# Kernel optimization log

Measured on AMD Instinct MI355X. Metric: run time of the kernel, lower is better.

The kernel has to match this reference:

```python
import jax, jax.numpy as jnp
import numpy as np

IN_C, HID, L, NN, BS, OUT = 32, 128, 4, 64, 512, 3
N = NN * BS  # total graph vertices
EPS_LN = 1e-5
EPS_SM = 1e-16  # PyG softmax eps


def setup_inputs() -> dict:
    key = jax.random.key(0)
    ks = jax.random.split(key, 16)
    E = 524288
    x = jax.random.normal(ks[0], (N, IN_C), dtype=jnp.float32)
    edge_index = jax.random.randint(ks[1], (2, E), 0, N, dtype=jnp.int64)
    s = 0.1
    # first GAT layer (in -> hidden)
    W0 = jax.random.normal(ks[2], (IN_C, HID), dtype=jnp.float32) * s
    att_src0 = jax.random.normal(ks[3], (HID,), dtype=jnp.float32) * s
    att_dst0 = jax.random.normal(ks[4], (HID,), dtype=jnp.float32) * s
    bias0 = jnp.zeros((HID,), dtype=jnp.float32)
    # residual GAT layers (hidden -> hidden), stacked over L
    W_res = jax.random.normal(ks[5], (L, HID, HID), dtype=jnp.float32) * s
    att_src_res = jax.random.normal(ks[6], (L, HID), dtype=jnp.float32) * s
    att_dst_res = jax.random.normal(ks[7], (L, HID), dtype=jnp.float32) * s
    bias_res = jnp.zeros((L, HID), dtype=jnp.float32)
    gamma = jnp.ones((L, HID), dtype=jnp.float32)
    beta = jnp.zeros((L, HID), dtype=jnp.float32)
    # per-node predictor heads
    W1p = jax.random.normal(ks[8], (NN, HID, HID // 2), dtype=jnp.float32) * s
    W2p = jax.random.normal(ks[9], (NN, HID // 2, OUT), dtype=jnp.float32) * s
    return {"x": x, "edge_index": edge_index, "W0": W0, "att_src0": att_src0,
            "att_dst0": att_dst0, "bias0": bias0, "W_res": W_res,
            "att_src_res": att_src_res, "att_dst_res": att_dst_res,
            "bias_res": bias_res, "gamma": gamma, "beta": beta,
            "W1p": W1p, "W2p": W2p}


def _gat(x, src, dst, W, a_src, a_dst, b):
    # PyG GATConv, heads=1, negative_slope=0.2, self-loops already appended
    h = x @ W                                   # [N, H]
    a_s = (h * a_src).sum(-1)                   # [N]
    a_d = (h * a_dst).sum(-1)                   # [N]
    e = jax.nn.leaky_relu(a_s[src] + a_d[dst], 0.2)   # [E]
    m = jax.ops.segment_max(e, dst, num_segments=N)
    e = jnp.exp(e - m[dst])
    z = jax.ops.segment_sum(e, dst, num_segments=N)
    alpha = e / (z[dst] + EPS_SM)               # [E]
    out = jax.ops.segment_sum(h[src] * alpha[:, None], dst, num_segments=N)
    return out + b


def _layernorm(x, g, b):
    mu = x.mean(-1, keepdims=True)
    var = ((x - mu) ** 2).mean(-1, keepdims=True)
    return (x - mu) * jax.lax.rsqrt(var + EPS_LN) * g + b


def reference(x, edge_index, W0, att_src0, att_dst0, bias0, W_res,
              att_src_res, att_dst_res, bias_res, gamma, beta, W1p, W2p):
    loops = jnp.arange(N, dtype=edge_index.dtype)
    src = jnp.concatenate([edge_index[0], loops])
    dst = jnp.concatenate([edge_index[1], loops])
    # first GAT + relu
    h = jax.nn.relu(_gat(x, src, dst, W0, att_src0, att_dst0, bias0))
    # res+ blocks: h = h + conv(dropout(act(norm(h))))  (dropout=identity, eval)
    for i in range(L):
        t = jax.nn.relu(_layernorm(h, gamma[i], beta[i]))
        t = _gat(t, src, dst, W_res[i], att_src_res[i], att_dst_res[i], bias_res[i])
        h = h + t
    h = jax.nn.relu(_layernorm(h, gamma[0], beta[0]))
    # per-node predictor heads
    h = h.reshape(NN, BS, HID)
    t = jax.nn.relu(jnp.einsum('nbh,nhk->nbk', h, W1p))
    logits = jnp.einsum('nbk,nko->nbo', t, W2p)
    return jax.nn.softmax(logits, axis=-1)   # softmax over class dim (dim=1 per node slice)
```

## Files before the change

### kernel.cpp

```cpp
#include <hip/hip_runtime.h>
#include <math.h>

#define NND   32768
#define HIDD  128
#define NHEAD 64
#define BSS   512
#define OUTC  3

typedef _Float16 half_t;
typedef __attribute__((ext_vector_type(8))) _Float16 half8;
typedef __attribute__((ext_vector_type(4))) float f32x4;

__global__ void count_kernel(const int* __restrict__ ei, int E,
                             int* __restrict__ counts, int* __restrict__ rank) {
    int j = blockIdx.x * 256 + threadIdx.x;
    int Etot = E + NND;
    if (j >= Etot) return;
    int dst = (j < E) ? ei[E + j] : (j - E);
    rank[j] = atomicAdd(&counts[dst], 1);
}

__global__ __launch_bounds__(1024) void scan_kernel(const int* __restrict__ counts,
                                                    int* __restrict__ off) {
    __shared__ int sums[1024];
    int tid = threadIdx.x;
    int base = tid * 32;
    int tmp[32];
    int run = 0;
#pragma unroll
    for (int i = 0; i < 8; ++i) {
        int4 c4 = *(const int4*)&counts[base + i * 4];
        tmp[i*4+0] = run; run += c4.x;
        tmp[i*4+1] = run; run += c4.y;
        tmp[i*4+2] = run; run += c4.z;
        tmp[i*4+3] = run; run += c4.w;
    }
    sums[tid] = run;
    __syncthreads();
    for (int d = 1; d < 1024; d <<= 1) {
        int v = (tid >= d) ? sums[tid - d] : 0;
        __syncthreads();
        sums[tid] += v;
        __syncthreads();
    }
    int ebase = (tid == 0) ? 0 : sums[tid - 1];
#pragma unroll
    for (int i = 0; i < 32; ++i) off[base + i] = ebase + tmp[i];
    if (tid == 1023) off[NND] = sums[1023];
}

__global__ void fill_kernel(const int* __restrict__ ei, int E,
                            const int* __restrict__ off, const int* __restrict__ rank,
                            int* __restrict__ csr_src) {
    int j = blockIdx.x * 256 + threadIdx.x;
    int Etot = E + NND;
    if (j >= Etot) return;
    int src, dst;
    if (j < E) { src = ei[j]; dst = ei[E + j]; }
    else       { src = j - E; dst = j - E; }
    csr_src[off[dst] + rank[j]] = src;
}

__global__ __launch_bounds__(256) void prep_kernel(const float* __restrict__ W_res,
                                                   const float* __restrict__ W1p,
                                                   half_t* __restrict__ Wh,
                                                   half_t* __restrict__ W1h) {
    __shared__ float tile[32][33];
    int b = blockIdx.x;
    const float* src; half_t* dst; int srcld, k0, n0;
    if (b < 64) {
        int l = b >> 4, t = b & 15;
        k0 = (t >> 2) * 32; n0 = (t & 3) * 32;
        src = W_res + (size_t)l * 128 * 128; srcld = 128;
        dst = Wh + (size_t)l * 128 * 128;
    } else {
        int bb = b - 64; int head = bb >> 3, t = bb & 7;
        k0 = (t >> 1) * 32; n0 = (t & 1) * 32;
        src = W1p + (size_t)head * 128 * 64; srcld = 64;
        dst = W1h + (size_t)head * 64 * 128;
    }
    int c = threadIdx.x & 31, r0 = threadIdx.x >> 5;
#pragma unroll
    for (int i = 0; i < 4; ++i) {
        int r = r0 + i * 8;
        tile[r][c] = src[(size_t)(k0 + r) * srcld + n0 + c];
    }
    __syncthreads();
#pragma unroll
    for (int i = 0; i < 4; ++i) {
        int rr = r0 + i * 8;
        dst[(size_t)(n0 + rr) * 128 + k0 + c] = (half_t)tile[c][rr];
    }
}

template <int K, int KT>
__global__ __launch_bounds__(256) void gemm_kernel(const float* __restrict__ X,
                                                   const float* __restrict__ W,
                                                   const float* __restrict__ att_src,
                                                   const float* __restrict__ att_dst,
                                                   half_t* __restrict__ Gh,
                                                   float* __restrict__ a_s,
                                                   float* __restrict__ a_d) {
    __shared__ float Ws[KT * HIDD];
    __shared__ float Xs[K * 32];
    int tid = threadIdx.x;
    int n0 = blockIdx.x * 32;
    for (int i = tid; i < 32 * K; i += 256) {
        int n = i / K, k = i - n * K;
        Xs[k * 32 + n] = X[(size_t)(n0 + n) * K + k];
    }
    int cg = (tid & 31) * 4;
    int ng = (tid >> 5) * 4;
    float acc[4][4] = {};
    for (int kt = 0; kt < K; kt += KT) {
        __syncthreads();
        for (int i = tid; i < KT * HIDD / 4; i += 256)
            ((float4*)Ws)[i] = ((const float4*)W)[(size_t)kt * (HIDD / 4) + i];
        __syncthreads();
#pragma unroll 4
        for (int k = 0; k < KT; ++k) {
            float4 wv = *(const float4*)&Ws[k * HIDD + cg];
            float4 xv = *(const float4*)&Xs[(kt + k) * 32 + ng];
            acc[0][0] += xv.x * wv.x; acc[0][1] += xv.x * wv.y; acc[0][2] += xv.x * wv.z; acc[0][3] += xv.x * wv.w;
            acc[1][0] += xv.y * wv.x; acc[1][1] += xv.y * wv.y; acc[1][2] += xv.y * wv.z; acc[1][3] += xv.y * wv.w;
            acc[2][0] += xv.z * wv.x; acc[2][1] += xv.z * wv.y; acc[2][2] += xv.z * wv.z; acc[2][3] += xv.z * wv.w;
            acc[3][0] += xv.w * wv.x; acc[3][1] += xv.w * wv.y; acc[3][2] += xv.w * wv.z; acc[3][3] += xv.w * wv.w;
        }
    }
    float4 asv = *(const float4*)&att_src[cg];
    float4 adv = *(const float4*)&att_dst[cg];
#pragma unroll
    for (int i = 0; i < 4; ++i) {
        int n = n0 + ng + i;
        union { int2 i2; half_t h[4]; } u;
        u.h[0] = (half_t)acc[i][0]; u.h[1] = (half_t)acc[i][1];
        u.h[2] = (half_t)acc[i][2]; u.h[3] = (half_t)acc[i][3];
        *(int2*)&Gh[(size_t)n * HIDD + cg] = u.i2;
        float ps = acc[i][0]*asv.x + acc[i][1]*asv.y + acc[i][2]*asv.z + acc[i][3]*asv.w;
        float pd = acc[i][0]*adv.x + acc[i][1]*adv.y + acc[i][2]*adv.z + acc[i][3]*adv.w;
#pragma unroll
        for (int o = 16; o; o >>= 1) { ps += __shfl_xor(ps, o); pd += __shfl_xor(pd, o); }
        if ((tid & 31) == 0) { a_s[n] = ps; a_d[n] = pd; }
    }
}

__global__ __launch_bounds__(256) void gemm_mfma_kernel(const half_t* __restrict__ Th,
                                                        const half_t* __restrict__ Whl,
                                                        const float* __restrict__ att_src,
                                                        const float* __restrict__ att_dst,
                                                        half_t* __restrict__ Gh,
                                                        float* __restrict__ a_s,
                                                        float* __restrict__ a_d) {
    __shared__ half_t Wt[128 * 136];
    __shared__ half_t OutT[64 * HIDD];
    int tid = threadIdx.x;
    int n0 = blockIdx.x * 64;
    for (int i = tid; i < 128 * 16; i += 256) {
        int n = i >> 4, c = i & 15;
        *(int4*)&Wt[n * 136 + c * 8] = *(const int4*)&Whl[(size_t)n * 128 + c * 8];
    }
    int wv = tid >> 6, lane = tid & 63;
    int q = lane >> 4, r15 = lane & 15;
    half8 afrag[4];
    int nodeA = n0 + wv * 16 + r15;
#pragma unroll
    for (int s = 0; s < 4; ++s)
        afrag[s] = *(const half8*)&Th[(size_t)nodeA * HIDD + s * 32 + q * 8];
    __syncthreads();
    f32x4 acc[8];
#pragma unroll
    for (int ct = 0; ct < 8; ++ct) {
        f32x4 c = {0.f, 0.f, 0.f, 0.f};
        int n = ct * 16 + r15;
#pragma unroll
        for (int s = 0; s < 4; ++s) {
            half8 b = *(const half8*)&Wt[n * 136 + s * 32 + q * 8];
            c = __builtin_amdgcn_mfma_f32_16x16x32_f16(afrag[s], b, c, 0, 0, 0);
        }
        acc[ct] = c;
    }
    float ps[4] = {0.f,0.f,0.f,0.f}, pd[4] = {0.f,0.f,0.f,0.f};
#pragma unroll
    for (int ct = 0; ct < 8; ++ct) {
        float av = att_src[ct * 16 + r15];
        float bv = att_dst[ct * 16 + r15];
#pragma unroll
        for (int r = 0; r < 4; ++r) {
            float v = acc[ct][r];
            ps[r] += v * av;
            pd[r] += v * bv;
            OutT[(wv * 16 + q * 4 + r) * HIDD + ct * 16 + r15] = (half_t)v;
        }
    }
#pragma unroll
    for (int o = 8; o; o >>= 1) {
#pragma unroll
        for (int r = 0; r < 4; ++r) { ps[r] += __shfl_xor(ps[r], o); pd[r] += __shfl_xor(pd[r], o); }
    }
    if (r15 == 0) {
#pragma unroll
        for (int r = 0; r < 4; ++r) {
            int node = n0 + wv * 16 + q * 4 + r;
            a_s[node] = ps[r];
            a_d[node] = pd[r];
        }
    }
    __syncthreads();
    const int4* srcp = (const int4*)OutT;
    int4* dstp = (int4*)&Gh[(size_t)n0 * HIDD];
    for (int i = tid; i < 64 * HIDD * 2 / 16; i += 256)
        dstp[i] = srcp[i];
}

__global__ __launch_bounds__(256) void agg_kernel(const half_t* __restrict__ Gh,
                                                  const float* __restrict__ a_s,
                                                  const float* __restrict__ a_dv,
                                                  const int* __restrict__ csr_src,
                                                  const int* __restrict__ off,
                                                  const float* __restrict__ bias,
                                                  const float* __restrict__ gamma,
                                                  const float* __restrict__ beta,
                                                  float* __restrict__ Hbuf,
                                                  half_t* __restrict__ Th,
                                                  int mode) {
    int d = (blockIdx.x * 256 + threadIdx.x) >> 6;
    int lane = threadIdx.x & 63;
    if (d >= NND) return;
    int q = lane >> 4, r15 = lane & 15;
    int beg = off[d], end = off[d + 1];
    float adv = a_dv[d];
    float pz = 0.f;
    float acc[8] = {0.f,0.f,0.f,0.f,0.f,0.f,0.f,0.f};
    for (int base = beg; base < end; base += 64) {
        int j = base + lane;
        int s = 0; float p = 0.f;
        if (j < end) {
            s = csr_src[j];
            float t = a_s[s] + adv;
            t = (t > 0.f) ? t : 0.2f * t;
            p = __expf(t);
        }
        pz += p;
        int cnt = end - base; if (cnt > 64) cnt = 64;
        for (int k4 = 0; k4 < cnt; k4 += 16) {
            int   s0 = __shfl(s, k4 + q);       float p0 = __shfl(p, k4 + q);
            int   s1 = __shfl(s, k4 + 4 + q);   float p1 = __shfl(p, k4 + 4 + q);
            int   s2 = __shfl(s, k4 + 8 + q);   float p2 = __shfl(p, k4 + 8 + q);
            int   s3 = __shfl(s, k4 + 12 + q);  float p3 = __shfl(p, k4 + 12 + q);
            half8 h0 = *(const half8*)&Gh[(size_t)s0 * HIDD + r15 * 8];
            half8 h1 = *(const half8*)&Gh[(size_t)s1 * HIDD + r15 * 8];
            half8 h2 = *(const half8*)&Gh[(size_t)s2 * HIDD + r15 * 8];
            half8 h3 = *(const half8*)&Gh[(size_t)s3 * HIDD + r15 * 8];
#pragma unroll
            for (int i = 0; i < 8; ++i) acc[i] += p0 * (float)h0[i];
#pragma unroll
            for (int i = 0; i < 8; ++i) acc[i] += p1 * (float)h1[i];
#pragma unroll
            for (int i = 0; i < 8; ++i) acc[i] += p2 * (float)h2[i];
#pragma unroll
            for (int i = 0; i < 8; ++i) acc[i] += p3 * (float)h3[i];
        }
    }
#pragma unroll
    for (int o = 32; o; o >>= 1) pz += __shfl_xor(pz, o);
#pragma unroll
    for (int i = 0; i < 8; ++i) {
        acc[i] += __shfl_xor(acc[i], 16);
        acc[i] += __shfl_xor(acc[i], 32);
    }
    float inv = 1.f / (pz + 1e-16f);
    float4 b0 = *(const float4*)&bias[r15 * 8];
    float4 b1 = *(const float4*)&bias[r15 * 8 + 4];
    float h[8];
    h[0] = acc[0]*inv + b0.x; h[1] = acc[1]*inv + b0.y; h[2] = acc[2]*inv + b0.z; h[3] = acc[3]*inv + b0.w;
    h[4] = acc[4]*inv + b1.x; h[5] = acc[5]*inv + b1.y; h[6] = acc[6]*inv + b1.z; h[7] = acc[7]*inv + b1.w;
    if (mode == 0) {
#pragma unroll
        for (int i = 0; i < 8; ++i) h[i] = fmaxf(h[i], 0.f);
    } else {
        float4 o0 = *(const float4*)&Hbuf[(size_t)d * HIDD + r15 * 8];
        float4 o1 = *(const float4*)&Hbuf[(size_t)d * HIDD + r15 * 8 + 4];
        h[0] += o0.x; h[1] += o0.y; h[2] += o0.z; h[3] += o0.w;
        h[4] += o1.x; h[5] += o1.y; h[6] += o1.z; h[7] += o1.w;
    }
    float sum = 0.f;
#pragma unroll
    for (int i = 0; i < 8; ++i) sum += h[i];
#pragma unroll
    for (int o = 8; o; o >>= 1) sum += __shfl_xor(sum, o);
    float mu = sum * (1.f / HIDD);
    float var = 0.f;
#pragma unroll
    for (int i = 0; i < 8; ++i) { float dx = h[i] - mu; var += dx * dx; }
#pragma unroll
    for (int o = 8; o; o >>= 1) var += __shfl_xor(var, o);
    float rs = rsqrtf(var * (1.f / HIDD) + 1e-5f);
    float4 g0 = *(const float4*)&gamma[r15 * 8];
    float4 g1 = *(const float4*)&gamma[r15 * 8 + 4];
    float4 bb0 = *(const float4*)&beta[r15 * 8];
    float4 bb1 = *(const float4*)&beta[r15 * 8 + 4];
    float gg[8] = {g0.x,g0.y,g0.z,g0.w,g1.x,g1.y,g1.z,g1.w};
    float be[8] = {bb0.x,bb0.y,bb0.z,bb0.w,bb1.x,bb1.y,bb1.z,bb1.w};
    if (q == 0) {
        *(float4*)&Hbuf[(size_t)d * HIDD + r15 * 8]     = make_float4(h[0], h[1], h[2], h[3]);
        *(float4*)&Hbuf[(size_t)d * HIDD + r15 * 8 + 4] = make_float4(h[4], h[5], h[6], h[7]);
        union { int4 v; half_t hh[8]; } u;
#pragma unroll
        for (int i = 0; i < 8; ++i)
            u.hh[i] = (half_t)fmaxf((h[i] - mu) * rs * gg[i] + be[i], 0.f);
        *(int4*)&Th[(size_t)d * HIDD + r15 * 8] = u.v;
    }
}

__global__ __launch_bounds__(256) void pred_kernel(const half_t* __restrict__ Th,
                                                   const half_t* __restrict__ W1h,
                                                   const float* __restrict__ W2p,
                                                   float* __restrict__ out) {
    __shared__ half_t W1t[64 * 136];
    __shared__ float W2s[64 * OUTC];
    int tid = threadIdx.x;
    int head = blockIdx.x >> 2;
    int part = blockIdx.x & 3;
    const half_t* W1g = W1h + (size_t)head * 64 * 128;
    for (int i = tid; i < 64 * 16; i += 256) {
        int n = i >> 4, c = i & 15;
        *(int4*)&W1t[n * 136 + c * 8] = *(const int4*)&W1g[(size_t)n * 128 + c * 8];
    }
    if (tid < 64 * OUTC) W2s[tid] = W2p[(size_t)head * 64 * OUTC + tid];
    __syncthreads();
    int wv = tid >> 6, lane = tid & 63;
    int q = lane >> 4, r15 = lane & 15;
#pragma unroll
    for (int t16 = 0; t16 < 2; ++t16) {
        int rowbase = part * 128 + wv * 32 + t16 * 16;
        int nodeA = head * BSS + rowbase + r15;
        half8 afrag[4];
#pragma unroll
        for (int s = 0; s < 4; ++s)
            afrag[s] = *(const half8*)&Th[(size_t)nodeA * HIDD + s * 32 + q * 8];
        float lg[3][4];
#pragma unroll
        for (int o = 0; o < 3; ++o)
#pragma unroll
            for (int r = 0; r < 4; ++r) lg[o][r] = 0.f;
#pragma unroll
        for (int ct = 0; ct < 4; ++ct) {
            f32x4 c = {0.f, 0.f, 0.f, 0.f};
#pragma unroll
            for (int s = 0; s < 4; ++s) {
                half8 b = *(const half8*)&W1t[(ct * 16 + r15) * 136 + s * 32 + q * 8];
                c = __builtin_amdgcn_mfma_f32_16x16x32_f16(afrag[s], b, c, 0, 0, 0);
            }
            float w2a = W2s[(ct * 16 + r15) * OUTC + 0];
            float w2b = W2s[(ct * 16 + r15) * OUTC + 1];
            float w2c = W2s[(ct * 16 + r15) * OUTC + 2];
#pragma unroll
            for (int r = 0; r < 4; ++r) {
                float t = fmaxf(c[r], 0.f);
                lg[0][r] += t * w2a;
                lg[1][r] += t * w2b;
                lg[2][r] += t * w2c;
            }
        }
#pragma unroll
        for (int o = 8; o; o >>= 1)
#pragma unroll
            for (int oo = 0; oo < 3; ++oo)
#pragma unroll
                for (int r = 0; r < 4; ++r) lg[oo][r] += __shfl_xor(lg[oo][r], o);
        if (r15 == 0) {
#pragma unroll
            for (int r = 0; r < 4; ++r) {
                int row = rowbase + q * 4 + r;
                float l0 = lg[0][r], l1 = lg[1][r], l2 = lg[2][r];
                float mx = fmaxf(l0, fmaxf(l1, l2));
                float e0 = __expf(l0 - mx), e1 = __expf(l1 - mx), e2 = __expf(l2 - mx);
                float inv = 1.f / (e0 + e1 + e2);
                float* op = out + (size_t)(head * BSS + row) * OUTC;
                op[0] = e0 * inv; op[1] = e1 * inv; op[2] = e2 * inv;
            }
        }
    }
}

extern "C" void kernel_launch(void* const* d_in, const int* in_sizes, int n_in,
                              void* d_out, int out_size, void* d_ws, size_t ws_size,
                              hipStream_t stream) {
    const float* x        = (const float*)d_in[0];
    const int*   ei       = (const int*)d_in[1];
    const float* W0       = (const float*)d_in[2];
    const float* att_src0 = (const float*)d_in[3];
    const float* att_dst0 = (const float*)d_in[4];
    const float* bias0    = (const float*)d_in[5];
    const float* W_res    = (const float*)d_in[6];
    const float* as_res   = (const float*)d_in[7];
    const float* ad_res   = (const float*)d_in[8];
    const float* b_res    = (const float*)d_in[9];
    const float* gamma    = (const float*)d_in[10];
    const float* beta     = (const float*)d_in[11];
    const float* W1p      = (const float*)d_in[12];
    const float* W2p      = (const float*)d_in[13];
    float* out = (float*)d_out;

    int E = in_sizes[1] / 2;
    int Etot = E + NND;

    char* p = (char*)d_ws;
    auto alloc = [&](size_t bytes) { void* r = (void*)p; p += (bytes + 255) & ~(size_t)255; return r; };
    int*    counts  = (int*)alloc((size_t)NND * 4);
    int*    off     = (int*)alloc((size_t)(NND + 1) * 4);
    int*    rank    = (int*)alloc((size_t)Etot * 4);
    int*    csr_src = (int*)alloc((size_t)Etot * 4);
    half_t* Gh      = (half_t*)alloc((size_t)NND * HIDD * 2);
    half_t* Th      = (half_t*)alloc((size_t)NND * HIDD * 2);
    float*  Hbuf    = (float*)alloc((size_t)NND * HIDD * 4);
    float*  a_s     = (float*)alloc((size_t)NND * 4);
    float*  a_d     = (float*)alloc((size_t)NND * 4);
    half_t* Wh      = (half_t*)alloc((size_t)4 * HIDD * HIDD * 2);
    half_t* W1h     = (half_t*)alloc((size_t)NHEAD * 64 * HIDD * 2);

    int egrid = (Etot + 255) / 256;

    hipMemsetAsync(counts, 0, (size_t)NND * 4, stream);
    count_kernel<<<egrid, 256, 0, stream>>>(ei, E, counts, rank);
    scan_kernel<<<1, 1024, 0, stream>>>(counts, off);
    fill_kernel<<<egrid, 256, 0, stream>>>(ei, E, off, rank, csr_src);
    prep_kernel<<<576, 256, 0, stream>>>(W_res, W1p, Wh, W1h);

    gemm_kernel<32, 32><<<NND / 32, 256, 0, stream>>>(x, W0, att_src0, att_dst0, Gh, a_s, a_d);
    agg_kernel<<<NND / 4, 256, 0, stream>>>(Gh, a_s, a_d, csr_src, off, bias0,
                                            gamma, beta, Hbuf, Th, 0);

    for (int i = 0; i < 4; ++i) {
        gemm_mfma_kernel<<<NND / 64, 256, 0, stream>>>(Th, Wh + (size_t)i * HIDD * HIDD,
                                                       as_res + i * HIDD, ad_res + i * HIDD,
                                                       Gh, a_s, a_d);
        int gi = (i < 3) ? (i + 1) : 0;
        agg_kernel<<<NND / 4, 256, 0, stream>>>(Gh, a_s, a_d, csr_src, off, b_res + i * HIDD,
                                                gamma + gi * HIDD, beta + gi * HIDD, Hbuf, Th, 1);
    }

    pred_kernel<<<dim3(NHEAD * 4), 256, 0, stream>>>(Th, W1h, W2p, out);
}
```

Before: 329.8 us.

## Aggregate before transform in GAT layers and precompute attention vectors W·att

Each GAT layer is reordered to aggregate the raw input features over neighbours first and then multiply by W, which is valid because the attention logits can be computed from the input using precomputed W·att vectors. For the first layer this gathers 32-wide fp16 inputs instead of 128-wide transformed features. LayerNorm, ReLU, the residual add and the next layer's attention logits are fused into the GEMM epilogue, and the predictor head is fused into the last GEMM. The fp16 input copy, the W·att products and the count zeroing move into a single prep kernel. The softmax is computed without max subtraction, which risks overflow for large logits, and fp16 rounding now happens at different points.

After: 302.5 us. 1.09x faster.

```diff
diff --git a/kernel.cpp b/kernel.cpp
--- a/kernel.cpp
+++ b/kernel.cpp
@@ -10,6 +10,94 @@
 typedef _Float16 half_t;
 typedef __attribute__((ext_vector_type(8))) _Float16 half8;
 typedef __attribute__((ext_vector_type(4))) float f32x4;
+
+__global__ __launch_bounds__(256) void prep_kernel(const float* __restrict__ W0,
+        const float* __restrict__ W_res, const float* __restrict__ W1p,
+        const float* __restrict__ as0, const float* __restrict__ ad0,
+        const float* __restrict__ as_res, const float* __restrict__ ad_res,
+        const float* __restrict__ x,
+        half_t* __restrict__ Wh, half_t* __restrict__ W1h, half_t* __restrict__ W0t,
+        float* __restrict__ wvec, half_t* __restrict__ xh, int* __restrict__ counts) {
+    int b = blockIdx.x, tid = threadIdx.x;
+    if (b < 64) {
+        __shared__ float tile[32][33];
+        int l = b >> 4, t = b & 15;
+        int k0 = (t >> 2) * 32, n0 = (t & 3) * 32;
+        const float* src = W_res + (size_t)l * 128 * 128;
+        half_t* dst = Wh + (size_t)l * 128 * 128;
+        int c = tid & 31, r0 = tid >> 5;
+#pragma unroll
+        for (int i = 0; i < 4; ++i) tile[r0 + i * 8][c] = src[(size_t)(k0 + r0 + i * 8) * 128 + n0 + c];
+        __syncthreads();
+#pragma unroll
+        for (int i = 0; i < 4; ++i) dst[(size_t)(n0 + r0 + i * 8) * 128 + k0 + c] = (half_t)tile[c][r0 + i * 8];
+    } else if (b < 576) {
+        __shared__ float tile[32][33];
+        int bb = b - 64, head = bb >> 3, t = bb & 7;
+        int k0 = (t >> 1) * 32, n0 = (t & 1) * 32;
+        const float* src = W1p + (size_t)head * 128 * 64;
+        half_t* dst = W1h + (size_t)head * 64 * 128;
+        int c = tid & 31, r0 = tid >> 5;
+#pragma unroll
+        for (int i = 0; i < 4; ++i) tile[r0 + i * 8][c] = src[(size_t)(k0 + r0 + i * 8) * 64 + n0 + c];
+        __syncthreads();
+#pragma unroll
+        for (int i = 0; i < 4; ++i) dst[(size_t)(n0 + r0 + i * 8) * 128 + k0 + c] = (half_t)tile[c][r0 + i * 8];
+    } else if (b == 576) {
+        __shared__ float t0[32][129];
+        for (int i = tid; i < 4096; i += 256) t0[i >> 7][i & 127] = W0[i];
+        __syncthreads();
+        for (int i = tid; i < 4096; i += 256) { int n = i >> 5, k = i & 31; W0t[n * 32 + k] = (half_t)t0[k][n]; }
+    } else if (b == 577) {
+        for (int task = tid; task < 1088; task += 256) {
+            const float* row; const float* att; int slot, sd;
+            if (task < 64) {
+                int k = task >> 1; sd = task & 1;
+                row = W0 + k * 128; att = sd ? ad0 : as0; slot = k;
+            } else {
+                int tt = task - 64; int l = 1 + tt / 256; int r = tt % 256;
+                int k = r >> 1; sd = r & 1;
+                row = W_res + (size_t)(l - 1) * 16384 + k * 128;
+                att = (sd ? ad_res : as_res) + (l - 1) * 128;
+                slot = l * 128 + k;
+            }
+            float s = 0.f;
+            for (int n = 0; n < 128; ++n) s += row[n] * att[n];
+            (sd ? wvec + 640 : wvec)[slot] = s;
+        }
+    } else if (b < 1090) {
+        int b2 = b - 578;
+        const float* xs = x + (size_t)b2 * 64 * 32;
+        half_t* xd = xh + (size_t)b2 * 64 * 32;
+        for (int i = tid; i < 1024; i += 256) {
+            float2 v = ((const float2*)xs)[i];
+            union { unsigned u; half_t h[2]; } cv;
+            cv.h[0] = (half_t)v.x; cv.h[1] = (half_t)v.y;
+            ((unsigned*)xd)[i] = cv.u;
+        }
+    } else {
+        int b3 = b - 1090;
+        ((int4*)counts)[b3 * 256 + tid] = make_int4(0, 0, 0, 0);
+    }
+}
+
+__global__ __launch_bounds__(256) void a0_kernel(const half_t* __restrict__ xh,
+                                                 const float* __restrict__ wvec,
+                                                 float* __restrict__ a_s, float* __restrict__ a_d) {
+    __shared__ float ws0[32], wd0[32];
+    int tid = threadIdx.x;
+    if (tid < 32) { ws0[tid] = wvec[tid]; wd0[tid] = wvec[640 + tid]; }
+    __syncthreads();
+    int g = blockIdx.x * 256 + tid;
+    int node = g >> 2, part = g & 3;
+    half8 xv = *(const half8*)&xh[(size_t)node * 32 + part * 8];
+    float s = 0.f, d2 = 0.f;
+#pragma unroll
+    for (int j = 0; j < 8; ++j) { float f = (float)xv[j]; s += f * ws0[part * 8 + j]; d2 += f * wd0[part * 8 + j]; }
+    s += __shfl_xor(s, 1); s += __shfl_xor(s, 2);
+    d2 += __shfl_xor(d2, 1); d2 += __shfl_xor(d2, 2);
+    if (part == 0) { a_s[node] = s; a_d[node] = d2; }
+}
 
 __global__ void count_kernel(const int* __restrict__ ei, int E,
                              int* __restrict__ counts, int* __restrict__ rank) {
@@ -61,171 +149,67 @@
     csr_src[off[dst] + rank[j]] = src;
 }
 
-__global__ __launch_bounds__(256) void prep_kernel(const float* __restrict__ W_res,
-                                                   const float* __restrict__ W1p,
-                                                   half_t* __restrict__ Wh,
-                                                   half_t* __restrict__ W1h) {
-    __shared__ float tile[32][33];
-    int b = blockIdx.x;
-    const float* src; half_t* dst; int srcld, k0, n0;
-    if (b < 64) {
-        int l = b >> 4, t = b & 15;
-        k0 = (t >> 2) * 32; n0 = (t & 3) * 32;
-        src = W_res + (size_t)l * 128 * 128; srcld = 128;
-        dst = Wh + (size_t)l * 128 * 128;
-    } else {
-        int bb = b - 64; int head = bb >> 3, t = bb & 7;
-        k0 = (t >> 1) * 32; n0 = (t & 1) * 32;
-        src = W1p + (size_t)head * 128 * 64; srcld = 64;
-        dst = W1h + (size_t)head * 64 * 128;
-    }
-    int c = threadIdx.x & 31, r0 = threadIdx.x >> 5;
-#pragma unroll
-    for (int i = 0; i < 4; ++i) {
-        int r = r0 + i * 8;
-        tile[r][c] = src[(size_t)(k0 + r) * srcld + n0 + c];
-    }
-    __syncthreads();
-#pragma unroll
-    for (int i = 0; i < 4; ++i) {
-        int rr = r0 + i * 8;
-        dst[(size_t)(n0 + rr) * 128 + k0 + c] = (half_t)tile[c][rr];
-    }
-}
-
-template <int K, int KT>
-__global__ __launch_bounds__(256) void gemm_kernel(const float* __restrict__ X,
-                                                   const float* __restrict__ W,
-                                                   const float* __restrict__ att_src,
-                                                   const float* __restrict__ att_dst,
-                                                   half_t* __restrict__ Gh,
-                                                   float* __restrict__ a_s,
-                                                   float* __restrict__ a_d) {
-    __shared__ float Ws[KT * HIDD];
-    __shared__ float Xs[K * 32];
-    int tid = threadIdx.x;
-    int n0 = blockIdx.x * 32;
-    for (int i = tid; i < 32 * K; i += 256) {
-        int n = i / K, k = i - n * K;
-        Xs[k * 32 + n] = X[(size_t)(n0 + n) * K + k];
-    }
-    int cg = (tid & 31) * 4;
-    int ng = (tid >> 5) * 4;
-    float acc[4][4] = {};
-    for (int kt = 0; kt < K; kt += KT) {
-        __syncthreads();
-        for (int i = tid; i < KT * HIDD / 4; i += 256)
-            ((float4*)Ws)[i] = ((const float4*)W)[(size_t)kt * (HIDD / 4) + i];
-        __syncthreads();
-#pragma unroll 4
-        for (int k = 0; k < KT; ++k) {
-            float4 wv = *(const float4*)&Ws[k * HIDD + cg];
-            float4 xv = *(const float4*)&Xs[(kt + k) * 32 + ng];
-            acc[0][0] += xv.x * wv.x; acc[0][1] += xv.x * wv.y; acc[0][2] += xv.x * wv.z; acc[0][3] += xv.x * wv.w;
-            acc[1][0] += xv.y * wv.x; acc[1][1] += xv.y * wv.y; acc[1][2] += xv.y * wv.z; acc[1][3] += xv.y * wv.w;
-            acc[2][0] += xv.z * wv.x; acc[2][1] += xv.z * wv.y; acc[2][2] += xv.z * wv.z; acc[2][3] += xv.z * wv.w;
-            acc[3][0] += xv.w * wv.x; acc[3][1] += xv.w * wv.y; acc[3][2] += xv.w * wv.z; acc[3][3] += xv.w * wv.w;
-        }
-    }
-    float4 asv = *(const float4*)&att_src[cg];
-    float4 adv = *(const float4*)&att_dst[cg];
-#pragma unroll
-    for (int i = 0; i < 4; ++i) {
-        int n = n0 + ng + i;
-        union { int2 i2; half_t h[4]; } u;
-        u.h[0] = (half_t)acc[i][0]; u.h[1] = (half_t)acc[i][1];
-        u.h[2] = (half_t)acc[i][2]; u.h[3] = (half_t)acc[i][3];
-        *(int2*)&Gh[(size_t)n * HIDD + cg] = u.i2;
-        float ps = acc[i][0]*asv.x + acc[i][1]*asv.y + acc[i][2]*asv.z + acc[i][3]*asv.w;
-        float pd = acc[i][0]*adv.x + acc[i][1]*adv.y + acc[i][2]*adv.z + acc[i][3]*adv.w;
-#pragma unroll
-        for (int o = 16; o; o >>= 1) { ps += __shfl_xor(ps, o); pd += __shfl_xor(pd, o); }
-        if ((tid & 31) == 0) { a_s[n] = ps; a_d[n] = pd; }
-    }
-}
-
-__global__ __launch_bounds__(256) void gemm_mfma_kernel(const half_t* __restrict__ Th,
-                                                        const half_t* __restrict__ Whl,
-                                                        const float* __restrict__ att_src,
-                                                        const float* __restrict__ att_dst,
-                                                        half_t* __restrict__ Gh,
-                                                        float* __restrict__ a_s,
-                                                        float* __restrict__ a_d) {
-    __shared__ half_t Wt[128 * 136];
-    __shared__ half_t OutT[64 * HIDD];
-    int tid = threadIdx.x;
-    int n0 = blockIdx.x * 64;
-    for (int i = tid; i < 128 * 16; i += 256) {
-        int n = i >> 4, c = i & 15;
-        *(int4*)&Wt[n * 136 + c * 8] = *(const int4*)&Whl[(size_t)n * 128 + c * 8];
-    }
-    int wv = tid >> 6, lane = tid & 63;
-    int q = lane >> 4, r15 = lane & 15;
-    half8 afrag[4];
-    int nodeA = n0 + wv * 16 + r15;
-#pragma unroll
-    for (int s = 0; s < 4; ++s)
-        afrag[s] = *(const half8*)&Th[(size_t)nodeA * HIDD + s * 32 + q * 8];
-    __syncthreads();
-    f32x4 acc[8];
-#pragma unroll
-    for (int ct = 0; ct < 8; ++ct) {
-        f32x4 c = {0.f, 0.f, 0.f, 0.f};
-        int n = ct * 16 + r15;
-#pragma unroll
-        for (int s = 0; s < 4; ++s) {
-            half8 b = *(const half8*)&Wt[n * 136 + s * 32 + q * 8];
-            c = __builtin_amdgcn_mfma_f32_16x16x32_f16(afrag[s], b, c, 0, 0, 0);
-        }
-        acc[ct] = c;
-    }
-    float ps[4] = {0.f,0.f,0.f,0.f}, pd[4] = {0.f,0.f,0.f,0.f};
-#pragma unroll
-    for (int ct = 0; ct < 8; ++ct) {
-        float av = att_src[ct * 16 + r15];
-        float bv = att_dst[ct * 16 + r15];
-#pragma unroll
-        for (int r = 0; r < 4; ++r) {
-            float v = acc[ct][r];
-            ps[r] += v * av;
-            pd[r] += v * bv;
-            OutT[(wv * 16 + q * 4 + r) * HIDD + ct * 16 + r15] = (half_t)v;
-        }
-    }
-#pragma unroll
-    for (int o = 8; o; o >>= 1) {
-#pragma unroll
-        for (int r = 0; r < 4; ++r) { ps[r] += __shfl_xor(ps[r], o); pd[r] += __shfl_xor(pd[r], o); }
-    }
-    if (r15 == 0) {
-#pragma unroll
-        for (int r = 0; r < 4; ++r) {
-            int node = n0 + wv * 16 + q * 4 + r;
-            a_s[node] = ps[r];
-            a_d[node] = pd[r];
-        }
-    }
-    __syncthreads();
-    const int4* srcp = (const int4*)OutT;
-    int4* dstp = (int4*)&Gh[(size_t)n0 * HIDD];
-    for (int i = tid; i < 64 * HIDD * 2 / 16; i += 256)
-        dstp[i] = srcp[i];
-}
-
-__global__ __launch_bounds__(256) void agg_kernel(const half_t* __restrict__ Gh,
-                                                  const float* __restrict__ a_s,
-                                                  const float* __restrict__ a_dv,
-                                                  const int* __restrict__ csr_src,
-                                                  const int* __restrict__ off,
-                                                  const float* __restrict__ bias,
-                                                  const float* __restrict__ gamma,
-                                                  const float* __restrict__ beta,
-                                                  float* __restrict__ Hbuf,
-                                                  half_t* __restrict__ Th,
-                                                  int mode) {
+__global__ __launch_bounds__(256) void agg0_kernel(const half_t* __restrict__ xh,
+        const float* __restrict__ a_s, const float* __restrict__ a_dv,
+        const int* __restrict__ csr_src, const int* __restrict__ off,
+        half_t* __restrict__ P) {
     int d = (blockIdx.x * 256 + threadIdx.x) >> 6;
     int lane = threadIdx.x & 63;
-    if (d >= NND) return;
+    int q = lane >> 4, r15 = lane & 15;
+    int beg = off[d], end = off[d + 1];
+    float adv = a_dv[d];
+    float pz = 0.f, a0 = 0.f, a1 = 0.f;
+    for (int base = beg; base < end; base += 64) {
+        int j = base + lane;
+        int s = 0; float p = 0.f;
+        if (j < end) {
+            s = csr_src[j];
+            float t = a_s[s] + adv;
+            t = (t > 0.f) ? t : 0.2f * t;
+            p = __expf(t);
+        }
+        pz += p;
+        int cnt = end - base; if (cnt > 64) cnt = 64;
+        int full = cnt & ~15;
+        int k4 = 0;
+        for (; k4 < full; k4 += 16) {
+            int s0 = __shfl(s, k4 + q);      float p0 = __shfl(p, k4 + q);
+            int s1 = __shfl(s, k4 + 4 + q);  float p1 = __shfl(p, k4 + 4 + q);
+            int s2 = __shfl(s, k4 + 8 + q);  float p2 = __shfl(p, k4 + 8 + q);
+            int s3 = __shfl(s, k4 + 12 + q); float p3 = __shfl(p, k4 + 12 + q);
+            union { unsigned u; half_t h[2]; } u0, u1, u2, u3;
+            u0.u = *(const unsigned*)&xh[(size_t)s0 * 32 + r15 * 2];
+            u1.u = *(const unsigned*)&xh[(size_t)s1 * 32 + r15 * 2];
+            u2.u = *(const unsigned*)&xh[(size_t)s2 * 32 + r15 * 2];
+            u3.u = *(const unsigned*)&xh[(size_t)s3 * 32 + r15 * 2];
+            a0 += p0 * (float)u0.h[0] + p1 * (float)u1.h[0] + p2 * (float)u2.h[0] + p3 * (float)u3.h[0];
+            a1 += p0 * (float)u0.h[1] + p1 * (float)u1.h[1] + p2 * (float)u2.h[1] + p3 * (float)u3.h[1];
+        }
+        for (; k4 < cnt; k4 += 4) {
+            int s0 = __shfl(s, k4 + q); float p0 = __shfl(p, k4 + q);
+            union { unsigned u; half_t h[2]; } u0;
+            u0.u = *(const unsigned*)&xh[(size_t)s0 * 32 + r15 * 2];
+            a0 += p0 * (float)u0.h[0]; a1 += p0 * (float)u0.h[1];
+        }
+    }
+#pragma unroll
+    for (int o = 32; o; o >>= 1) pz += __shfl_xor(pz, o);
+    a0 += __shfl_xor(a0, 16); a0 += __shfl_xor(a0, 32);
+    a1 += __shfl_xor(a1, 16); a1 += __shfl_xor(a1, 32);
+    if (q == 0) {
+        float inv = 1.f / (pz + 1e-16f);
+        union { unsigned u; half_t h[2]; } w;
+        w.h[0] = (half_t)(a0 * inv); w.h[1] = (half_t)(a1 * inv);
+        *(unsigned*)&P[(size_t)d * 32 + r15 * 2] = w.u;
+    }
+}
+
+__global__ __launch_bounds__(256) void agg_kernel(const half_t* __restrict__ F,
+        const float* __restrict__ a_s, const float* __restrict__ a_dv,
+        const int* __restrict__ csr_src, const int* __restrict__ off,
+        half_t* __restrict__ P) {
+    int d = (blockIdx.x * 256 + threadIdx.x) >> 6;
+    int lane = threadIdx.x & 63;
     int q = lane >> 4, r15 = lane & 15;
     int beg = off[d], end = off[d + 1];
     float adv = a_dv[d];
@@ -242,15 +226,17 @@
         }
         pz += p;
         int cnt = end - base; if (cnt > 64) cnt = 64;
-        for (int k4 = 0; k4 < cnt; k4 += 16) {
-            int   s0 = __shfl(s, k4 + q);       float p0 = __shfl(p, k4 + q);
-            int   s1 = __shfl(s, k4 + 4 + q);   float p1 = __shfl(p, k4 + 4 + q);
-            int   s2 = __shfl(s, k4 + 8 + q);   float p2 = __shfl(p, k4 + 8 + q);
-            int   s3 = __shfl(s, k4 + 12 + q);  float p3 = __shfl(p, k4 + 12 + q);
-            half8 h0 = *(const half8*)&Gh[(size_t)s0 * HIDD + r15 * 8];
-            half8 h1 = *(const half8*)&Gh[(size_t)s1 * HIDD + r15 * 8];
-            half8 h2 = *(const half8*)&Gh[(size_t)s2 * HIDD + r15 * 8];
-            half8 h3 = *(const half8*)&Gh[(size_t)s3 * HIDD + r15 * 8];
+        int full = cnt & ~15;
+        int k4 = 0;
+        for (; k4 < full; k4 += 16) {
+            int s0 = __shfl(s, k4 + q);      float p0 = __shfl(p, k4 + q);
+            int s1 = __shfl(s, k4 + 4 + q);  float p1 = __shfl(p, k4 + 4 + q);
+            int s2 = __shfl(s, k4 + 8 + q);  float p2 = __shfl(p, k4 + 8 + q);
+            int s3 = __shfl(s, k4 + 12 + q); float p3 = __shfl(p, k4 + 12 + q);
+            half8 h0 = *(const half8*)&F[(size_t)s0 * HIDD + r15 * 8];
+            half8 h1 = *(const half8*)&F[(size_t)s1 * HIDD + r15 * 8];
+            half8 h2 = *(const half8*)&F[(size_t)s2 * HIDD + r15 * 8];
+            half8 h3 = *(const half8*)&F[(size_t)s3 * HIDD + r15 * 8];
 #pragma unroll
             for (int i = 0; i < 8; ++i) acc[i] += p0 * (float)h0[i];
 #pragma unroll
@@ -259,6 +245,12 @@
             for (int i = 0; i < 8; ++i) acc[i] += p2 * (float)h2[i];
 #pragma unroll
             for (int i = 0; i < 8; ++i) acc[i] += p3 * (float)h3[i];
+        }
+        for (; k4 < cnt; k4 += 4) {
+            int s0 = __shfl(s, k4 + q); float p0 = __shfl(p, k4 + q);
+            half8 h0 = *(const half8*)&F[(size_t)s0 * HIDD + r15 * 8];
+#pragma unroll
+            for (int i = 0; i < 8; ++i) acc[i] += p0 * (float)h0[i];
         }
     }
 #pragma unroll
@@ -268,117 +260,240 @@
         acc[i] += __shfl_xor(acc[i], 16);
         acc[i] += __shfl_xor(acc[i], 32);
     }
-    float inv = 1.f / (pz + 1e-16f);
-    float4 b0 = *(const float4*)&bias[r15 * 8];
-    float4 b1 = *(const float4*)&bias[r15 * 8 + 4];
-    float h[8];
-    h[0] = acc[0]*inv + b0.x; h[1] = acc[1]*inv + b0.y; h[2] = acc[2]*inv + b0.z; h[3] = acc[3]*inv + b0.w;
-    h[4] = acc[4]*inv + b1.x; h[5] = acc[5]*inv + b1.y; h[6] = acc[6]*inv + b1.z; h[7] = acc[7]*inv + b1.w;
-    if (mode == 0) {
-#pragma unroll
-        for (int i = 0; i < 8; ++i) h[i] = fmaxf(h[i], 0.f);
-    } else {
-        float4 o0 = *(const float4*)&Hbuf[(size_t)d * HIDD + r15 * 8];
-        float4 o1 = *(const float4*)&Hbuf[(size_t)d * HIDD + r15 * 8 + 4];
-        h[0] += o0.x; h[1] += o0.y; h[2] += o0.z; h[3] += o0.w;
-        h[4] += o1.x; h[5] += o1.y; h[6] += o1.z; h[7] += o1.w;
-    }
-    float sum = 0.f;
-#pragma unroll
-    for (int i = 0; i < 8; ++i) sum += h[i];
-#pragma unroll
-    for (int o = 8; o; o >>= 1) sum += __shfl_xor(sum, o);
-    float mu = sum * (1.f / HIDD);
-    float var = 0.f;
-#pragma unroll
-    for (int i = 0; i < 8; ++i) { float dx = h[i] - mu; var += dx * dx; }
-#pragma unroll
-    for (int o = 8; o; o >>= 1) var += __shfl_xor(var, o);
-    float rs = rsqrtf(var * (1.f / HIDD) + 1e-5f);
-    float4 g0 = *(const float4*)&gamma[r15 * 8];
-    float4 g1 = *(const float4*)&gamma[r15 * 8 + 4];
-    float4 bb0 = *(const float4*)&beta[r15 * 8];
-    float4 bb1 = *(const float4*)&beta[r15 * 8 + 4];
-    float gg[8] = {g0.x,g0.y,g0.z,g0.w,g1.x,g1.y,g1.z,g1.w};
-    float be[8] = {bb0.x,bb0.y,bb0.z,bb0.w,bb1.x,bb1.y,bb1.z,bb1.w};
     if (q == 0) {
-        *(float4*)&Hbuf[(size_t)d * HIDD + r15 * 8]     = make_float4(h[0], h[1], h[2], h[3]);
-        *(float4*)&Hbuf[(size_t)d * HIDD + r15 * 8 + 4] = make_float4(h[4], h[5], h[6], h[7]);
+        float inv = 1.f / (pz + 1e-16f);
         union { int4 v; half_t hh[8]; } u;
 #pragma unroll
-        for (int i = 0; i < 8; ++i)
-            u.hh[i] = (half_t)fmaxf((h[i] - mu) * rs * gg[i] + be[i], 0.f);
-        *(int4*)&Th[(size_t)d * HIDD + r15 * 8] = u.v;
-    }
-}
-
-__global__ __launch_bounds__(256) void pred_kernel(const half_t* __restrict__ Th,
-                                                   const half_t* __restrict__ W1h,
-                                                   const float* __restrict__ W2p,
-                                                   float* __restrict__ out) {
-    __shared__ half_t W1t[64 * 136];
-    __shared__ float W2s[64 * OUTC];
+        for (int i = 0; i < 8; ++i) u.hh[i] = (half_t)(acc[i] * inv);
+        *(int4*)&P[(size_t)d * HIDD + r15 * 8] = u.v;
+    }
+}
+
+template <int K, bool RES>
+__global__ __launch_bounds__(256) void gemm_kernel(const half_t* __restrict__ P,
+        const half_t* __restrict__ Whl, const float* __restrict__ bias,
+        float* __restrict__ Hbuf, half_t* __restrict__ Th,
+        const float* __restrict__ gamma, const float* __restrict__ beta,
+        const float* __restrict__ wsn, const float* __restrict__ wdn,
+        float* __restrict__ a_s, float* __restrict__ a_d) {
+    constexpr int KP = K + 8;
+    __shared__ half_t Wt[128 * KP];
+    __shared__ half_t OutT[64 * HIDD];
     int tid = threadIdx.x;
-    int head = blockIdx.x >> 2;
-    int part = blockIdx.x & 3;
-    const half_t* W1g = W1h + (size_t)head * 64 * 128;
-    for (int i = tid; i < 64 * 16; i += 256) {
-        int n = i >> 4, c = i & 15;
-        *(int4*)&W1t[n * 136 + c * 8] = *(const int4*)&W1g[(size_t)n * 128 + c * 8];
-    }
-    if (tid < 64 * OUTC) W2s[tid] = W2p[(size_t)head * 64 * OUTC + tid];
-    __syncthreads();
+    int n0 = blockIdx.x * 64;
+    for (int i = tid; i < 128 * (K / 8); i += 256) {
+        int n = i / (K / 8), c = i % (K / 8);
+        *(int4*)&Wt[n * KP + c * 8] = *(const int4*)&Whl[(size_t)n * K + c * 8];
+    }
     int wv = tid >> 6, lane = tid & 63;
     int q = lane >> 4, r15 = lane & 15;
-#pragma unroll
-    for (int t16 = 0; t16 < 2; ++t16) {
-        int rowbase = part * 128 + wv * 32 + t16 * 16;
-        int nodeA = head * BSS + rowbase + r15;
-        half8 afrag[4];
-#pragma unroll
-        for (int s = 0; s < 4; ++s)
-            afrag[s] = *(const half8*)&Th[(size_t)nodeA * HIDD + s * 32 + q * 8];
-        float lg[3][4];
-#pragma unroll
-        for (int o = 0; o < 3; ++o)
-#pragma unroll
-            for (int r = 0; r < 4; ++r) lg[o][r] = 0.f;
-#pragma unroll
-        for (int ct = 0; ct < 4; ++ct) {
-            f32x4 c = {0.f, 0.f, 0.f, 0.f};
-#pragma unroll
-            for (int s = 0; s < 4; ++s) {
-                half8 b = *(const half8*)&W1t[(ct * 16 + r15) * 136 + s * 32 + q * 8];
-                c = __builtin_amdgcn_mfma_f32_16x16x32_f16(afrag[s], b, c, 0, 0, 0);
-            }
-            float w2a = W2s[(ct * 16 + r15) * OUTC + 0];
-            float w2b = W2s[(ct * 16 + r15) * OUTC + 1];
-            float w2c = W2s[(ct * 16 + r15) * OUTC + 2];
-#pragma unroll
-            for (int r = 0; r < 4; ++r) {
-                float t = fmaxf(c[r], 0.f);
-                lg[0][r] += t * w2a;
-                lg[1][r] += t * w2b;
-                lg[2][r] += t * w2c;
-            }
-        }
-#pragma unroll
-        for (int o = 8; o; o >>= 1)
-#pragma unroll
-            for (int oo = 0; oo < 3; ++oo)
-#pragma unroll
-                for (int r = 0; r < 4; ++r) lg[oo][r] += __shfl_xor(lg[oo][r], o);
-        if (r15 == 0) {
-#pragma unroll
-            for (int r = 0; r < 4; ++r) {
-                int row = rowbase + q * 4 + r;
-                float l0 = lg[0][r], l1 = lg[1][r], l2 = lg[2][r];
-                float mx = fmaxf(l0, fmaxf(l1, l2));
-                float e0 = __expf(l0 - mx), e1 = __expf(l1 - mx), e2 = __expf(l2 - mx);
-                float inv = 1.f / (e0 + e1 + e2);
-                float* op = out + (size_t)(head * BSS + row) * OUTC;
-                op[0] = e0 * inv; op[1] = e1 * inv; op[2] = e2 * inv;
-            }
+    half8 afrag[K / 32];
+    int nodeA = n0 + wv * 16 + r15;
+#pragma unroll
+    for (int s = 0; s < K / 32; ++s)
+        afrag[s] = *(const half8*)&P[(size_t)nodeA * K + s * 32 + q * 8];
+    __syncthreads();
+    f32x4 acc[8];
+#pragma unroll
+    for (int ct = 0; ct < 8; ++ct) {
+        f32x4 c = {0.f, 0.f, 0.f, 0.f};
+#pragma unroll
+        for (int s = 0; s < K / 32; ++s) {
+            half8 bfrag = *(const half8*)&Wt[(ct * 16 + r15) * KP + s * 32 + q * 8];
+            c = __builtin_amdgcn_mfma_f32_16x16x32_f16(afrag[s], bfrag, c, 0, 0, 0);
+        }
+        acc[ct] = c;
+    }
+    int nodeD = n0 + wv * 16 + q * 4;
+    float v[8][4];
+#pragma unroll
+    for (int ct = 0; ct < 8; ++ct) {
+        int ch = ct * 16 + r15;
+        float bv = bias[ch];
+#pragma unroll
+        for (int r = 0; r < 4; ++r) {
+            float x2 = acc[ct][r] + bv;
+            if (RES) x2 += Hbuf[(size_t)(nodeD + r) * HIDD + ch];
+            else     x2 = fmaxf(x2, 0.f);
+            v[ct][r] = x2;
+            Hbuf[(size_t)(nodeD + r) * HIDD + ch] = x2;
+        }
+    }
+    float sum[4] = {0.f,0.f,0.f,0.f};
+#pragma unroll
+    for (int ct = 0; ct < 8; ++ct)
+#pragma unroll
+        for (int r = 0; r < 4; ++r) sum[r] += v[ct][r];
+#pragma unroll
+    for (int o = 8; o; o >>= 1)
+#pragma unroll
+        for (int r = 0; r < 4; ++r) sum[r] += __shfl_xor(sum[r], o);
+    float mu[4], var[4] = {0.f,0.f,0.f,0.f};
+#pragma unroll
+    for (int r = 0; r < 4; ++r) mu[r] = sum[r] * (1.f / HIDD);
+#pragma unroll
+    for (int ct = 0; ct < 8; ++ct)
+#pragma unroll
+        for (int r = 0; r < 4; ++r) { float dx = v[ct][r] - mu[r]; var[r] += dx * dx; }
+#pragma unroll
+    for (int o = 8; o; o >>= 1)
+#pragma unroll
+        for (int r = 0; r < 4; ++r) var[r] += __shfl_xor(var[r], o);
+    float rs[4];
+#pragma unroll
+    for (int r = 0; r < 4; ++r) rs[r] = rsqrtf(var[r] * (1.f / HIDD) + 1e-5f);
+    float asn[4] = {0.f,0.f,0.f,0.f}, adn[4] = {0.f,0.f,0.f,0.f};
+#pragma unroll
+    for (int ct = 0; ct < 8; ++ct) {
+        int ch = ct * 16 + r15;
+        float g = gamma[ch], be = beta[ch], wsv = wsn[ch], wdv = wdn[ch];
+#pragma unroll
+        for (int r = 0; r < 4; ++r) {
+            float t = fmaxf((v[ct][r] - mu[r]) * rs[r] * g + be, 0.f);
+            OutT[(wv * 16 + q * 4 + r) * HIDD + ch] = (half_t)t;
+            asn[r] += t * wsv;
+            adn[r] += t * wdv;
+        }
+    }
+#pragma unroll
+    for (int o = 8; o; o >>= 1)
+#pragma unroll
+        for (int r = 0; r < 4; ++r) { asn[r] += __shfl_xor(asn[r], o); adn[r] += __shfl_xor(adn[r], o); }
+    if (r15 == 0) {
+#pragma unroll
+        for (int r = 0; r < 4; ++r) { a_s[nodeD + r] = asn[r]; a_d[nodeD + r] = adn[r]; }
+    }
+    __syncthreads();
+    const int4* srcp = (const int4*)OutT;
+    int4* dstp = (int4*)&Th[(size_t)n0 * HIDD];
+    for (int i = tid; i < 64 * HIDD * 2 / 16; i += 256)
+        dstp[i] = srcp[i];
+}
+
+__global__ __launch_bounds__(256) void gemm_last_kernel(const half_t* __restrict__ P,
+        const half_t* __restrict__ Whl, const float* __restrict__ bias,
+        const float* __restrict__ Hbuf,
+        const float* __restrict__ gamma, const float* __restrict__ beta,
+        const half_t* __restrict__ W1h, const float* __restrict__ W2p,
+        float* __restrict__ out) {
+    __shared__ half_t Wt[128 * 136];
+    __shared__ half_t OutT[64 * HIDD];
+    int tid = threadIdx.x;
+    int n0 = blockIdx.x * 64;
+    for (int i = tid; i < 128 * 16; i += 256) {
+        int n = i >> 4, c = i & 15;
+        *(int4*)&Wt[n * 136 + c * 8] = *(const int4*)&Whl[(size_t)n * 128 + c * 8];
+    }
+    int wv = tid >> 6, lane = tid & 63;
+    int q = lane >> 4, r15 = lane & 15;
+    half8 afrag[4];
+    int nodeA = n0 + wv * 16 + r15;
+#pragma unroll
+    for (int s = 0; s < 4; ++s)
+        afrag[s] = *(const half8*)&P[(size_t)nodeA * HIDD + s * 32 + q * 8];
+    __syncthreads();
+    f32x4 acc[8];
+#pragma unroll
+    for (int ct = 0; ct < 8; ++ct) {
+        f32x4 c = {0.f, 0.f, 0.f, 0.f};
+#pragma unroll
+        for (int s = 0; s < 4; ++s) {
+            half8 bfrag = *(const half8*)&Wt[(ct * 16 + r15) * 136 + s * 32 + q * 8];
+            c = __builtin_amdgcn_mfma_f32_16x16x32_f16(afrag[s], bfrag, c, 0, 0, 0);
+        }
+        acc[ct] = c;
+    }
+    int nodeD = n0 + wv * 16 + q * 4;
+    float v[8][4];
+#pragma unroll
+    for (int ct = 0; ct < 8; ++ct) {
+        int ch = ct * 16 + r15;
+        float bv = bias[ch];
+#pragma unroll
+        for (int r = 0; r < 4; ++r)
+            v[ct][r] = acc[ct][r] + bv + Hbuf[(size_t)(nodeD + r) * HIDD + ch];
+    }
+    float sum[4] = {0.f,0.f,0.f,0.f};
+#pragma unroll
+    for (int ct = 0; ct < 8; ++ct)
+#pragma unroll
+        for (int r = 0; r < 4; ++r) sum[r] += v[ct][r];
+#pragma unroll
+    for (int o = 8; o; o >>= 1)
+#pragma unroll
+        for (int r = 0; r < 4; ++r) sum[r] += __shfl_xor(sum[r], o);
+    float mu[4], var[4] = {0.f,0.f,0.f,0.f};
+#pragma unroll
+    for (int r = 0; r < 4; ++r) mu[r] = sum[r] * (1.f / HIDD);
+#pragma unroll
+    for (int ct = 0; ct < 8; ++ct)
+#pragma unroll
+        for (int r = 0; r < 4; ++r) { float dx = v[ct][r] - mu[r]; var[r] += dx * dx; }
+#pragma unroll
+    for (int o = 8; o; o >>= 1)
+#pragma unroll
+        for (int r = 0; r < 4; ++r) var[r] += __shfl_xor(var[r], o);
+    float rs[4];
+#pragma unroll
+    for (int r = 0; r < 4; ++r) rs[r] = rsqrtf(var[r] * (1.f / HIDD) + 1e-5f);
+#pragma unroll
+    for (int ct = 0; ct < 8; ++ct) {
+        int ch = ct * 16 + r15;
+        float g = gamma[ch], be = beta[ch];
+#pragma unroll
+        for (int r = 0; r < 4; ++r) {
+            float t = fmaxf((v[ct][r] - mu[r]) * rs[r] * g + be, 0.f);
+            OutT[(wv * 16 + q * 4 + r) * HIDD + ch] = (half_t)t;
+        }
+    }
+    __syncthreads();
+    int head = n0 >> 9;
+    const half_t* W1g = W1h + (size_t)head * 64 * 128;
+    half8 pa[4];
+#pragma unroll
+    for (int s = 0; s < 4; ++s)
+        pa[s] = *(const half8*)&OutT[(wv * 16 + r15) * HIDD + s * 32 + q * 8];
+    float lg[3][4];
+#pragma unroll
+    for (int o = 0; o < 3; ++o)
+#pragma unroll
+        for (int r = 0; r < 4; ++r) lg[o][r] = 0.f;
+#pragma unroll
+    for (int ct2 = 0; ct2 < 4; ++ct2) {
+        int n2 = ct2 * 16 + r15;
+        f32x4 c = {0.f, 0.f, 0.f, 0.f};
+#pragma unroll
+        for (int s = 0; s < 4; ++s) {
+            half8 bfrag = *(const half8*)&W1g[(size_t)n2 * 128 + s * 32 + q * 8];
+            c = __builtin_amdgcn_mfma_f32_16x16x32_f16(pa[s], bfrag, c, 0, 0, 0);
+        }
+        float w2a = W2p[(size_t)head * 192 + n2 * 3 + 0];
+        float w2b = W2p[(size_t)head * 192 + n2 * 3 + 1];
+        float w2c = W2p[(size_t)head * 192 + n2 * 3 + 2];
+#pragma unroll
+        for (int r = 0; r < 4; ++r) {
+            float t = fmaxf(c[r], 0.f);
+            lg[0][r] += t * w2a;
+            lg[1][r] += t * w2b;
+            lg[2][r] += t * w2c;
+        }
+    }
+#pragma unroll
+    for (int o = 8; o; o >>= 1)
+#pragma unroll
+        for (int oo = 0; oo < 3; ++oo)
+#pragma unroll
+            for (int r = 0; r < 4; ++r) lg[oo][r] += __shfl_xor(lg[oo][r], o);
+    if (r15 == 0) {
+#pragma unroll
+        for (int r = 0; r < 4; ++r) {
+            int node = nodeD + r;
+            float l0 = lg[0][r], l1 = lg[1][r], l2 = lg[2][r];
+            float mx = fmaxf(l0, fmaxf(l1, l2));
+            float e0 = __expf(l0 - mx), e1 = __expf(l1 - mx), e2 = __expf(l2 - mx);
+            float inv = 1.f / (e0 + e1 + e2);
+            float* op = out + (size_t)node * OUTC;
+            op[0] = e0 * inv; op[1] = e1 * inv; op[2] = e2 * inv;
         }
     }
 }
@@ -411,34 +526,39 @@
     int*    off     = (int*)alloc((size_t)(NND + 1) * 4);
     int*    rank    = (int*)alloc((size_t)Etot * 4);
     int*    csr_src = (int*)alloc((size_t)Etot * 4);
-    half_t* Gh      = (half_t*)alloc((size_t)NND * HIDD * 2);
+    half_t* xh      = (half_t*)alloc((size_t)NND * 32 * 2);
+    half_t* Pbuf    = (half_t*)alloc((size_t)NND * HIDD * 2);
     half_t* Th      = (half_t*)alloc((size_t)NND * HIDD * 2);
     float*  Hbuf    = (float*)alloc((size_t)NND * HIDD * 4);
     float*  a_s     = (float*)alloc((size_t)NND * 4);
     float*  a_d     = (float*)alloc((size_t)NND * 4);
     half_t* Wh      = (half_t*)alloc((size_t)4 * HIDD * HIDD * 2);
     half_t* W1h     = (half_t*)alloc((size_t)NHEAD * 64 * HIDD * 2);
+    half_t* W0t     = (half_t*)alloc((size_t)HIDD * 32 * 2);
+    float*  wvec    = (float*)alloc((size_t)1280 * 4);
 
     int egrid = (Etot + 255) / 256;
 
-    hipMemsetAsync(counts, 0, (size_t)NND * 4, stream);
+    prep_kernel<<<1122, 256, 0, stream>>>(W0, W_res, W1p, att_src0, att_dst0,
+                                          as_res, ad_res, x, Wh, W1h, W0t, wvec, xh, counts);
+    a0_kernel<<<512, 256, 0, stream>>>(xh, wvec, a_s, a_d);
     count_kernel<<<egrid, 256, 0, stream>>>(ei, E, counts, rank);
     scan_kernel<<<1, 1024, 0, stream>>>(counts, off);
     fill_kernel<<<egrid, 256, 0, stream>>>(ei, E, off, rank, csr_src);
-    prep_kernel<<<576, 256, 0, stream>>>(W_res, W1p, Wh, W1h);
-
-    gemm_kernel<32, 32><<<NND / 32, 256, 0, stream>>>(x, W0, att_src0, att_dst0, Gh, a_s, a_d);
-    agg_kernel<<<NND / 4, 256, 0, stream>>>(Gh, a_s, a_d, csr_src, off, bias0,
-                                            gamma, beta, Hbuf, Th, 0);
-
-    for (int i = 0; i < 4; ++i) {
-        gemm_mfma_kernel<<<NND / 64, 256, 0, stream>>>(Th, Wh + (size_t)i * HIDD * HIDD,
-                                                       as_res + i * HIDD, ad_res + i * HIDD,
-                                                       Gh, a_s, a_d);
-        int gi = (i < 3) ? (i + 1) : 0;
-        agg_kernel<<<NND / 4, 256, 0, stream>>>(Gh, a_s, a_d, csr_src, off, b_res + i * HIDD,
-                                                gamma + gi * HIDD, beta + gi * HIDD, Hbuf, Th, 1);
-    }
-
-    pred_kernel<<<dim3(NHEAD * 4), 256, 0, stream>>>(Th, W1h, W2p, out);
-}
+
+    agg0_kernel<<<NND / 4, 256, 0, stream>>>(xh, a_s, a_d, csr_src, off, Pbuf);
+    gemm_kernel<32, false><<<NND / 64, 256, 0, stream>>>(Pbuf, W0t, bias0, Hbuf, Th,
+        gamma, beta, wvec + 128, wvec + 640 + 128, a_s, a_d);
+
+    for (int i = 0; i < 3; ++i) {
+        agg_kernel<<<NND / 4, 256, 0, stream>>>(Th, a_s, a_d, csr_src, off, Pbuf);
+        gemm_kernel<128, true><<<NND / 64, 256, 0, stream>>>(Pbuf, Wh + (size_t)i * 16384,
+            b_res + i * HIDD, Hbuf, Th,
+            gamma + (i + 1) * HIDD, beta + (i + 1) * HIDD,
+            wvec + (i + 2) * 128, wvec + 640 + (i + 2) * 128, a_s, a_d);
+    }
+
+    agg_kernel<<<NND / 4, 256, 0, stream>>>(Th, a_s, a_d, csr_src, off, Pbuf);
+    gemm_last_kernel<<<NND / 64, 256, 0, stream>>>(Pbuf, Wh + (size_t)3 * 16384,
+        b_res + 3 * HIDD, Hbuf, gamma, beta, W1h, W2p, out);
+}
```
